# Optimization experiments

Measured on AMD Instinct MI355X. Metric: run time of the kernel, lower is better.

Reference implementation:

```python
import jax, jax.numpy as jnp
from jax import lax
import numpy as np

# 8-neighbor topology from the original module
TOPO = np.array([[0, 1], [1, 1], [1, 0], [1, -1], [0, -1], [-1, -1], [-1, 0], [-1, 1]])
EPS = 1e-5


def conv(x, w, stride=1, pad=0, groups=1):
    # NCHW / OIHW convolution, no bias (module uses bias=False everywhere)
    return lax.conv_general_dilated(
        x, w, (stride, stride), [(pad, pad), (pad, pad)],
        feature_group_count=groups,
        dimension_numbers=('NCHW', 'OIHW', 'NCHW'))


def bn(x, g, b):
    # training-mode BatchNorm2d (batch statistics, biased variance)
    m = jnp.mean(x, axis=(0, 2, 3), keepdims=True)
    v = jnp.var(x, axis=(0, 2, 3), keepdims=True)
    return g[None, :, None, None] * (x - m) * lax.rsqrt(v + EPS) + b[None, :, None, None]


def setup_inputs() -> dict:
    key = jax.random.key(0)
    ks = jax.random.split(key, 12)
    B, D, NC, H, W = 8, 6, 48, 256, 256
    s = 0.1
    w = lambda k, shape: jax.random.normal(k, shape, jnp.float32) * s
    return dict(
        x=jax.random.normal(ks[0], (B, D, H, W), jnp.float32),
        # compenv_conv: Conv(D->NC,1) BN tanh Conv(NC->1,1)
        ce_w1=w(ks[1], (NC, D, 1, 1)), ce_g=jnp.ones(NC), ce_b=jnp.zeros(NC),
        ce_w2=w(ks[2], (1, NC, 1, 1)),
        # merge_change_determinant: funnel(ConvT(10->NC,3) tanh Conv(NC->NC,3) tanh) BN tanh Conv(NC->1,2,s2) sigmoid
        # ConvT stride-1 k3 expressed as pad-2 conv with conv-equivalent kernel
        md_ct=w(ks[3], (NC, 10, 3, 3)), md_c1=w(ks[4], (NC, NC, 3, 3)),
        md_g=jnp.ones(NC), md_b=jnp.zeros(NC), md_c2=w(ks[5], (1, NC, 2, 2)),
        # cell_merge: Conv(D->NC,2,s2,g3) BN tanh funnel(ConvT(NC->NC,3,g3) tanh Conv(NC->D,3,g3) tanh)
        cm_w1=w(ks[6], (NC, D // 3, 2, 2)), cm_g=jnp.ones(NC), cm_b=jnp.zeros(NC),
        cm_ct=w(ks[7], (NC, NC // 3, 3, 3)), cm_c2=w(ks[8], (D, NC // 3, 3, 3)),
        # born: Conv(D->NC,1) BN tanh Conv(NC->D,1)
        bo_w1=w(ks[9], (NC, D, 1, 1)), bo_g=jnp.ones(NC), bo_b=jnp.zeros(NC),
        bo_w2=w(ks[10], (D, NC, 1, 1)),
    )


def reference(x, ce_w1, ce_g, ce_b, ce_w2, md_ct, md_c1, md_g, md_b, md_c2,
              cm_w1, cm_g, cm_b, cm_ct, cm_c2, bo_w1, bo_g, bo_b, bo_w2):
    # ---- compenv: per-direction roll + 1x1conv/BN/tanh/1x1conv (BN stats per direction, as in torch) ----
    env = []
    for k in range(8):
        t = jnp.roll(x, int(TOPO[k, 0]), axis=3)      # roll_right along W
        t = jnp.roll(t, int(-TOPO[k, 1]), axis=2)     # roll_down along H
        h = jnp.tanh(bn(conv(t, ce_w1), ce_g, ce_b))
        env.append(conv(h, ce_w2))                    # [B,1,H,W]
    ENV = jnp.concatenate(env, axis=1)                # [B,8,H,W]

    # ---- merge change determinant ----
    te = jnp.concatenate([x[:, :2], ENV], axis=1)     # [B,10,H,W]
    h = jnp.tanh(conv(te, md_ct, pad=2))              # ConvT k3 s1 == pad-2 conv -> [B,NC,H+2,W+2]
    h = jnp.tanh(conv(h, md_c1))                      # -> [B,NC,H,W]
    h = jnp.tanh(bn(h, md_g, md_b))
    CHANGE = jax.nn.sigmoid(conv(h, md_c2, stride=2))  # [B,1,H/2,W/2]

    # ---- cell merge ----
    h = jnp.tanh(bn(conv(x, cm_w1, stride=2, groups=3), cm_g, cm_b))  # [B,NC,H/2,W/2]
    h = jnp.tanh(conv(h, cm_ct, pad=2, groups=3))
    xm = jnp.tanh(conv(h, cm_c2, groups=3))           # [B,D,H/2,W/2]

    # ---- born + blend ----
    born = conv(jnp.tanh(bn(conv(xm, bo_w1), bo_g, bo_b)), bo_w2)
    out = xm * (1.0 - CHANGE) + CHANGE * born
    out = jnp.concatenate([jax.nn.sigmoid(out[:, :3]), out[:, 3:]], axis=1)
    return out
```

## Files before the change

### kernel.cpp

```cpp
#include <hip/hip_runtime.h>
#include <stdint.h>

typedef unsigned short ushort_t;

#define B8  8
#define D6  6
#define NC  48
#define HH  256
#define WW  256
#define HWp 65536
#define H2  128
#define HW2 16384

__device__ __constant__ int c_T0[8] = {0,1,1,1,0,-1,-1,-1};
__device__ __constant__ int c_T1[8] = {1,1,0,-1,-1,-1,0,1};

__device__ inline float bf2f(ushort_t u){ union{unsigned int i; float f;} w; w.i = ((unsigned int)u)<<16; return w.f; }
__device__ inline ushort_t f2bf(float f){ union{float f; unsigned int i;} w; w.f=f; unsigned int xx=w.i;
  return (ushort_t)((xx + 0x7fffu + ((xx>>16)&1u)) >> 16); }
__device__ inline float tanhf_(float x){ float e=__expf(2.f*x); return 1.f - 2.f/(e+1.f); }
__device__ inline float sigm_(float x){ return 1.f/(1.f+__expf(-x)); }
__device__ inline float ldg_(const void* p, size_t i, int isbf){
  return isbf ? bf2f(((const ushort_t*)p)[i]) : ((const float*)p)[i];
}

typedef short short8 __attribute__((ext_vector_type(8)));
typedef float f4 __attribute__((ext_vector_type(4)));
typedef ushort_t us4 __attribute__((ext_vector_type(4)));
typedef ushort_t us8 __attribute__((ext_vector_type(8)));
union AB { short8 s; us4 h[2]; us8 u; };

__global__ __launch_bounds__(256) void k_detect(const ushort_t* x, float* flag){
  int t=threadIdx.x; int cnt=0;
  for(int i=t;i<4096;i+=256){
    ushort_t u=x[2*i];
    int e=(u>>7)&0xff;
    if(e>=100 && e<=150) cnt++;
  }
  for(int o=32;o;o>>=1) cnt+=__shfl_down(cnt,o,64);
  __shared__ int sh4[4];
  if((t&63)==0) sh4[t>>6]=cnt;
  __syncthreads();
  if(t==0){ int tot=sh4[0]+sh4[1]+sh4[2]+sh4[3]; flag[0] = (tot>=2048)?1.f:0.f; }
}

struct WC { const ushort_t* src[10]; int off[10]; int n[10]; };

__global__ __launch_bounds__(256) void k_wcvt(WC wc, float* dst, const float* dfl){
  int isbf = dfl[0]>0.5f;
  int t = blockIdx.y; int n = wc.n[t]; const ushort_t* s = wc.src[t]; float* d = dst + wc.off[t];
  for(int i = blockIdx.x*256 + threadIdx.x; i < n; i += gridDim.x*256)
    d[i] = isbf ? bf2f(s[i]) : ((const float*)s)[i];
}

__global__ __launch_bounds__(256) void k_wprep(const float* w2src, const float* w1src,
                                               ushort_t* wb2, ushort_t* wb1){
  int t = blockIdx.x*256+threadIdx.x;
  if(t<3456){
    int lane=t&63; int rest=t>>6;
    int ks=rest&1; int g=rest>>1; int tap=g%9; int nt=g/9;
    int oc=nt*16+(lane&15); int icb=ks*32+((lane>>4)*8);
    #pragma unroll
    for(int j=0;j<8;j++){
      int ic=icb+j;
      float v = (ic<48) ? w2src[(oc*48+ic)*9+tap] : 0.f;
      wb2[(size_t)t*8+j]=f2bf(v);
    }
  } else if(t<5184){
    int tt=t-3456; int lane=tt&63; int g=tt>>6; int tap=g%9; int nt=g/9;
    int oc=nt*16+(lane&15); int icb=(lane>>4)*8;
    #pragma unroll
    for(int j=0;j<8;j++){
      int ic=icb+j;
      float v = (ic<10) ? w1src[(oc*10+ic)*9+tap] : 0.f;
      wb1[(size_t)tt*8+j]=f2bf(v);
    }
  }
}

__global__ __launch_bounds__(256) void k_mom(const void* src, const float* dfl, int isbfc,
                                             int sh, int npix, float* out){
  int isbf = dfl ? (dfl[0]>0.5f) : isbfc;
  float vals[27];
  #pragma unroll
  for(int i=0;i<27;i++) vals[i]=0.f;
  int stride = gridDim.x*256;
  int msk = (1<<sh)-1;
  for(int p = blockIdx.x*256+threadIdx.x; p < npix; p += stride){
    int b = p >> sh; int hw = p & msk;
    float v[6];
    #pragma unroll
    for(int d=0; d<6; d++){
      size_t idx = (((size_t)(b*6+d))<<sh) + hw;
      v[d] = ldg_(src, idx, isbf);
    }
    int q=6;
    #pragma unroll
    for(int d=0;d<6;d++){
      vals[d]+=v[d];
      #pragma unroll
      for(int e=d;e<6;e++){ vals[q] += v[d]*v[e]; q++; }
    }
  }
  __shared__ float red[4][27];
  int wid=threadIdx.x>>6, lane=threadIdx.x&63;
  #pragma unroll
  for(int i=0;i<27;i++){
    float v=vals[i];
    for(int o=32;o;o>>=1) v+=__shfl_down(v,o,64);
    if(lane==0) red[wid][i]=v;
  }
  __syncthreads();
  if(threadIdx.x<27)
    atomicAdd(&out[threadIdx.x],
      red[0][threadIdx.x]+red[1][threadIdx.x]+red[2][threadIdx.x]+red[3][threadIdx.x]);
}

__global__ __launch_bounds__(64) void k_msb(const float* mom, const float* W1,
      const void* g, const void* b, const float* dfl, float invN, float* scale, float* bias){
  int c = threadIdx.x; if(c>=NC) return;
  int isbf = dfl[0]>0.5f;
  const int st[6]={0,6,11,15,18,20};
  float wr[6];
  #pragma unroll
  for(int d=0;d<6;d++) wr[d]=W1[c*6+d];
  float mean=0.f;
  #pragma unroll
  for(int d=0;d<6;d++) mean += wr[d]*mom[d];
  mean *= invN;
  float e2=0.f;
  #pragma unroll
  for(int d=0;d<6;d++){
    #pragma unroll
    for(int e=d;e<6;e++){
      float mm = mom[6 + st[d] + (e-d)];
      e2 += wr[d]*wr[e]*((e==d)?1.f:2.f)*mm;
    }
  }
  e2 *= invN;
  float var = e2 - mean*mean;
  float sc = ldg_(g,c,isbf) * rsqrtf(var + 1e-5f);
  scale[c]=sc; bias[c]= ldg_(b,c,isbf) - sc*mean;
}

__global__ __launch_bounds__(256) void k_env(const void* x, const float* dfl,
      const float* w1, const float* w2, const float* sc, const float* bi, float* e){
  int isbf = dfl[0]>0.5f;
  int p = blockIdx.x*256+threadIdx.x;
  int b = p >> 16; int hw = p & 65535;
  float v[6];
  #pragma unroll
  for(int d=0; d<6; d++) v[d]=ldg_(x,(size_t)(b*6+d)*HWp + hw, isbf);
  float acc=0.f;
  for(int c=0;c<NC;c++){
    float y=0.f;
    #pragma unroll
    for(int d=0;d<6;d++) y += w1[c*6+d]*v[d];
    acc += w2[c]*tanhf_(sc[c]*y + bi[c]);
  }
  e[(size_t)b*HWp + hw]=acc;
}

__global__ __launch_bounds__(256,3) void k_md(const void* x, const float* dfl, const float* e,
      const ushort_t* wb1, const ushort_t* wb2, ushort_t* h2t, float* stats){
  __shared__ __attribute__((aligned(16))) ushort_t te[6400];
  __shared__ __attribute__((aligned(16))) ushort_t h1t[19488];
  __shared__ float red[4][3][16][2];
  int isbf = dfl[0]>0.5f;
  int b = blockIdx.y;
  int ti = blockIdx.x>>4, tj = blockIdx.x&15;
  int i0 = ti*16, j0 = tj*16;
  int lane = threadIdx.x&63, w = threadIdx.x>>6;
  int n = lane&15, quad = lane>>4;
  {
    us8 z;
    #pragma unroll
    for(int j=0;j<8;j++) z[j]=0;
    us8* tp=(us8*)te;
    for(int idx=threadIdx.x; idx<800; idx+=256) tp[idx]=z;
    for(int idx=threadIdx.x; idx<336; idx+=256) *(us8*)&h1t[idx*58+48]=z;
  }
  __syncthreads();
  for(int idx=threadIdx.x; idx<4000; idx+=256){
    int pix = idx/10, ic = idx-pix*10;
    int r = pix/20, c = pix-r*20;
    int gy = i0-2+r, gx = j0-2+c;
    float v = 0.f;
    if(gy>=0 && gy<HH && gx>=0 && gx<WW){
      if(ic<2) v = ldg_(x, ((size_t)(b*6+ic)*HH + gy)*WW + gx, isbf);
      else { int k=ic-2;
        int yy=(gy + c_T1[k]) & 255; int xx=(gx - c_T0[k]) & 255;
        v = e[((size_t)b*HH + yy)*WW + xx]; }
    }
    te[pix*16+ic]=f2bf(v);
  }
  __syncthreads();
  {
    int qoff = (quad&1)*8;
    for(int mt=w; mt<21; mt+=4){
      int p = mt*16 + n;
      int pr = p/18, pc = p-pr*18;
      f4 hacc[3];
      #pragma unroll
      for(int nt=0;nt<3;nt++) hacc[nt]=(f4){0.f,0.f,0.f,0.f};
      #pragma unroll
      for(int tap=0; tap<9; tap++){
        int ki=tap/3, kj=tap%3;
        AB a; a.u = *(const us8*)&te[((pr+ki)*20 + pc+kj)*16 + qoff];
        #pragma unroll
        for(int nt=0;nt<3;nt++){
          AB Bf; Bf.u = *(const us8*)&wb1[((size_t)((nt*9+tap)*64+lane))*8];
          hacc[nt] = __builtin_amdgcn_mfma_f32_16x16x32_bf16(a.s, Bf.s, hacc[nt], 0,0,0);
        }
      }
      int pd = mt*16 + quad*4;
      #pragma unroll
      for(int nt=0;nt<3;nt++){
        #pragma unroll
        for(int r=0;r<4;r++)
          h1t[(pd+r)*58 + nt*16 + n] = f2bf(tanhf_(hacc[nt][r]));
      }
    }
  }
  __syncthreads();
  f4 acc[4][3];
  #pragma unroll
  for(int a=0;a<4;a++)
    #pragma unroll
    for(int c=0;c<3;c++) acc[a][c]=(f4){0.f,0.f,0.f,0.f};
  int q1off = 32 + ((quad<2) ? quad*8 : 16);
  #pragma unroll
  for(int tap=0; tap<9; tap++){
    int ki=tap/3, kj=tap%3;
    AB Bf[3][2];
    #pragma unroll
    for(int nt=0;nt<3;nt++)
      #pragma unroll
      for(int ks=0;ks<2;ks++)
        Bf[nt][ks].u = *(const us8*)&wb2[((size_t)(((nt*9+tap)*2+ks)*64+lane))*8];
    #pragma unroll
    for(int yy=0; yy<4; yy++){
      int y = w*4 + yy;
      int base = ((y+ki)*18 + n + kj)*58;
      AB a0, a1;
      a0.u = *(const us8*)&h1t[base + quad*8];
      a1.u = *(const us8*)&h1t[base + q1off];
      #pragma unroll
      for(int nt=0;nt<3;nt++){
        acc[yy][nt] = __builtin_amdgcn_mfma_f32_16x16x32_bf16(a0.s, Bf[nt][0].s, acc[yy][nt], 0,0,0);
        acc[yy][nt] = __builtin_amdgcn_mfma_f32_16x16x32_bf16(a1.s, Bf[nt][1].s, acc[yy][nt], 0,0,0);
      }
    }
  }
  float s[3]={0.f,0.f,0.f}, q[3]={0.f,0.f,0.f};
  size_t tilebase = ((size_t)(b*256 + blockIdx.x))*48*256;
  #pragma unroll
  for(int yy=0;yy<4;yy++){
    #pragma unroll
    for(int nt=0;nt<3;nt++){
      int oc = nt*16 + n;
      size_t base = tilebase + (size_t)oc*256 + (w*4+yy)*16 + quad*4;
      us4 u;
      #pragma unroll
      for(int r=0;r<4;r++){
        float v=tanhf_(acc[yy][nt][r]);
        u[r]=f2bf(v);
        float vb=bf2f(u[r]);
        s[nt]+=vb; q[nt]+=vb*vb;
      }
      *(us4*)&h2t[base] = u;
    }
  }
  #pragma unroll
  for(int nt=0;nt<3;nt++){
    s[nt]+=__shfl_xor(s[nt],16,64); s[nt]+=__shfl_xor(s[nt],32,64);
    q[nt]+=__shfl_xor(q[nt],16,64); q[nt]+=__shfl_xor(q[nt],32,64);
  }
  if(quad==0){
    #pragma unroll
    for(int nt=0;nt<3;nt++){ red[w][nt][n][0]=s[nt]; red[w][nt][n][1]=q[nt]; }
  }
  __syncthreads();
  if(threadIdx.x<48){
    int oc=threadIdx.x; int nt=oc>>4, nn=oc&15;
    float S=red[0][nt][nn][0]+red[1][nt][nn][0]+red[2][nt][nn][0]+red[3][nt][nn][0];
    float Q=red[0][nt][nn][1]+red[1][nt][nn][1]+red[2][nt][nn][1]+red[3][nt][nn][1];
    atomicAdd(&stats[2*oc],S); atomicAdd(&stats[2*oc+1],Q);
  }
}

__global__ __launch_bounds__(256) void k_cstat(const float* srcf, const ushort_t* srch, int isbf,
      int C, int HWn, int Bn, int S, float* stats){
  int c = blockIdx.x % C; int s = blockIdx.x / C;
  float sum=0.f, sq=0.f;
  for(int b=0;b<Bn;b++){
    size_t base=((size_t)b*C+c)*HWn;
    for(int i=s*256+threadIdx.x; i<HWn; i+=S*256){
      float v = isbf ? bf2f(srch[base+i]) : srcf[base+i];
      sum+=v; sq+=v*v;
    }
  }
  for(int o=32;o;o>>=1){ sum+=__shfl_down(sum,o,64); sq+=__shfl_down(sq,o,64); }
  __shared__ float ls[4], lq[4];
  int wid=threadIdx.x>>6;
  if((threadIdx.x&63)==0){ ls[wid]=sum; lq[wid]=sq; }
  __syncthreads();
  if(threadIdx.x==0){
    atomicAdd(&stats[2*c],   ls[0]+ls[1]+ls[2]+ls[3]);
    atomicAdd(&stats[2*c+1], lq[0]+lq[1]+lq[2]+lq[3]);
  }
}

__global__ __launch_bounds__(64) void k_csb(const float* stats, const void* g, const void* b,
      const float* dfl, float invN, float* scale, float* bias){
  int c=threadIdx.x; if(c>=NC) return;
  int isbf = dfl[0]>0.5f;
  float mean=stats[2*c]*invN; float var=stats[2*c+1]*invN - mean*mean;
  float s=ldg_(g,c,isbf)*rsqrtf(var+1e-5f);
  scale[c]=s; bias[c]=ldg_(b,c,isbf)-s*mean;
}

__global__ __launch_bounds__(256) void k_change(const ushort_t* h2t,
      const float* wc2, const float* sc, const float* bi, float* CH){
  int tile = blockIdx.x;
  int b = tile>>8; int rest = tile&255; int ti = rest>>4, tj = rest&15;
  int t = threadIdx.x;
  int pix = t&63, icq = t>>6;
  int oi = pix>>3, oj = pix&7;
  const ushort_t* tp = &h2t[(size_t)tile*48*256];
  float acc = 0.f;
  #pragma unroll
  for(int icl=0; icl<12; icl++){
    int ic = icq*12 + icl;
    float s = sc[ic], tb = bi[ic];
    const ushort_t* cp = tp + ic*256 + (2*oi)*16 + 2*oj;
    acc += tanhf_(s*bf2f(cp[0 ])+tb)*wc2[ic*4+0];
    acc += tanhf_(s*bf2f(cp[1 ])+tb)*wc2[ic*4+1];
    acc += tanhf_(s*bf2f(cp[16])+tb)*wc2[ic*4+2];
    acc += tanhf_(s*bf2f(cp[17])+tb)*wc2[ic*4+3];
  }
  __shared__ float rr[256];
  rr[icq*64+pix] = acc;
  __syncthreads();
  if(t<64){
    float v = rr[t]+rr[64+t]+rr[128+t]+rr[192+t];
    int i = ti*8 + (t>>3), j = tj*8 + (t&7);
    CH[((size_t)b<<14) + i*128 + j] = sigm_(v);
  }
}

__global__ __launch_bounds__(256) void k_cm1(const void* x, const float* dfl, const float* w, ushort_t* t1){
  int isbf = dfl[0]>0.5f;
  int p=blockIdx.x*256+threadIdx.x;
  int b=p>>14; int rem=p&16383; int i=rem>>7; int j=rem&127;
  float v[6][2][2];
  #pragma unroll
  for(int d=0;d<6;d++)
    #pragma unroll
    for(int ki=0;ki<2;ki++)
      #pragma unroll
      for(int kj=0;kj<2;kj++)
        v[d][ki][kj]=ldg_(x, ((size_t)(b*6+d)*HH + 2*i+ki)*WW + 2*j+kj, isbf);
  for(int oc=0;oc<NC;oc++){
    int g=oc>>4;
    float a=0.f;
    #pragma unroll
    for(int icl=0;icl<2;icl++)
      #pragma unroll
      for(int ki=0;ki<2;ki++)
        #pragma unroll
        for(int kj=0;kj<2;kj++)
          a += v[2*g+icl][ki][kj]*w[((oc*2+icl)*2+ki)*2+kj];
    t1[((size_t)(b*NC+oc)*HW2) + rem]=f2bf(a);
  }
}

__global__ __launch_bounds__(256) void k_cm2(const ushort_t* t1, const float* sc, const float* bi,
        const float* wct, float* t2){
  __shared__ float as[16][20][21];
  int b=blockIdx.y, g=blockIdx.z;
  int ti=blockIdx.x/9, tj=blockIdx.x%9;
  int i0=ti*16, j0=tj*16;
  int ty=threadIdx.x>>4, tx=threadIdx.x&15;
  for(int idx=threadIdx.x; idx<6400; idx+=256){
    int i=idx/400; int rem=idx-i*400; int r=rem/20; int cc=rem-r*20;
    int cg=g*16+i;
    int y=i0-2+r, xx=j0-2+cc;
    float v=0.f;
    if(y>=0 && y<H2 && xx>=0 && xx<H2)
      v = tanhf_(sc[cg]*bf2f(t1[((size_t)(b*NC+cg)*H2 + y)*H2 + xx]) + bi[cg]);
    as[i][r][cc]=v;
  }
  __syncthreads();
  float acc[16];
  #pragma unroll
  for(int o=0;o<16;o++) acc[o]=0.f;
  for(int i=0;i<16;i++){
    float p[3][3];
    #pragma unroll
    for(int ki=0;ki<3;ki++)
      #pragma unroll
      for(int kj=0;kj<3;kj++) p[ki][kj]=as[i][ty+ki][tx+kj];
    #pragma unroll
    for(int o=0;o<16;o++){
      const float* wp=&wct[((size_t)(g*16+o)*16+i)*9];
      float a=0.f;
      #pragma unroll
      for(int q=0;q<9;q++) a += p[q/3][q%3]*wp[q];
      acc[o]+=a;
    }
  }
  int ii=i0+ty, jj=j0+tx;
  if(ii<130 && jj<130){
    #pragma unroll
    for(int o=0;o<16;o++)
      t2[((size_t)(b*NC+g*16+o)*130 + ii)*130 + jj]=tanhf_(acc[o]);
  }
}

__global__ __launch_bounds__(256) void k_cm3(const float* t2, const float* w, float* xm){
  __shared__ float ts[16][18][20];
  int b=blockIdx.y, g=blockIdx.z;
  int ti=blockIdx.x>>3, tj=blockIdx.x&7;
  int i0=ti*16, j0=tj*16;
  int ty=threadIdx.x>>4, tx=threadIdx.x&15;
  for(int idx=threadIdx.x; idx<16*18*18; idx+=256){
    int i=idx/324; int rem=idx-i*324; int r=rem/18; int cc=rem-r*18;
    int cg=g*16+i;
    ts[i][r][cc]=t2[((size_t)(b*NC+cg)*130 + i0+r)*130 + j0+cc];
  }
  __syncthreads();
  float acc[2]={0.f,0.f};
  for(int icl=0;icl<16;icl++){
    float p[3][3];
    #pragma unroll
    for(int ki=0;ki<3;ki++)
      #pragma unroll
      for(int kj=0;kj<3;kj++) p[ki][kj]=ts[icl][ty+ki][tx+kj];
    #pragma unroll
    for(int ol=0;ol<2;ol++){
      int oc=2*g+ol;
      const float* wp=&w[((size_t)oc*16+icl)*9];
      float a=0.f;
      #pragma unroll
      for(int q=0;q<9;q++) a += p[q/3][q%3]*wp[q];
      acc[ol]+=a;
    }
  }
  int ii=i0+ty, jj=j0+tx;
  #pragma unroll
  for(int ol=0;ol<2;ol++)
    xm[((size_t)(b*6+2*g+ol)*H2 + ii)*H2 + jj]=tanhf_(acc[ol]);
}

__global__ __launch_bounds__(256) void k_final(const float* xm, const float* CH, const float* w1,
      const float* w2, const float* sc, const float* bi, const float* dfl, void* outp){
  int isbf = dfl[0]>0.5f;
  int p=blockIdx.x*256+threadIdx.x;
  int b=p>>14; int rem=p&16383;
  float v[6];
  #pragma unroll
  for(int d=0;d<6;d++) v[d]=xm[((size_t)(b*6+d)*HW2)+rem];
  float born[6]={0.f,0.f,0.f,0.f,0.f,0.f};
  for(int c=0;c<NC;c++){
    float y=0.f;
    #pragma unroll
    for(int d=0;d<6;d++) y+=w1[c*6+d]*v[d];
    float a=tanhf_(sc[c]*y+bi[c]);
    #pragma unroll
    for(int d=0;d<6;d++) born[d]+=w2[d*NC+c]*a;
  }
  float C=CH[p];
  #pragma unroll
  for(int d=0;d<6;d++){
    float o=v[d]*(1.f-C)+C*born[d];
    if(d<3) o=sigm_(o);
    size_t id=((size_t)(b*6+d)*HW2)+rem;
    if(isbf) ((ushort_t*)outp)[id]=f2bf(o); else ((float*)outp)[id]=o;
  }
}

extern "C" void kernel_launch(void* const* d_in, const int* in_sizes, int n_in,
                              void* d_out, int out_size, void* d_ws, size_t ws_size,
                              hipStream_t stream){
  (void)in_sizes; (void)n_in; (void)out_size; (void)ws_size;
  const ushort_t* x    = (const ushort_t*)d_in[0];
  const ushort_t* cew1 = (const ushort_t*)d_in[1];
  const void*     ceg  = d_in[2];
  const void*     ceb  = d_in[3];
  const ushort_t* cew2 = (const ushort_t*)d_in[4];
  const ushort_t* mdct = (const ushort_t*)d_in[5];
  const ushort_t* mdc1 = (const ushort_t*)d_in[6];
  const void*     mdg  = d_in[7];
  const void*     mdb  = d_in[8];
  const ushort_t* mdc2 = (const ushort_t*)d_in[9];
  const ushort_t* cmw1 = (const ushort_t*)d_in[10];
  const void*     cmg  = d_in[11];
  const void*     cmb  = d_in[12];
  const ushort_t* cmct = (const ushort_t*)d_in[13];
  const ushort_t* cmc2 = (const ushort_t*)d_in[14];
  const ushort_t* bow1 = (const ushort_t*)d_in[15];
  const void*     bog  = d_in[16];
  const void*     bob  = d_in[17];
  const ushort_t* bow2 = (const ushort_t*)d_in[18];
  float* ws = (float*)d_ws;

  const long OW_mdct=0, OW_mdc1=4320, OW_cew1=25056, OW_cew2=25344, OW_mdc2=25392,
             OW_cmw1=25584, OW_cmct=25968, OW_cmc2=32880, OW_bow1=33744, OW_bow2=34032;
  const long OFF_STATS=34320;
  const long ST_xmom=OFF_STATS+0,  ST_cesc=OFF_STATS+64,  ST_cebi=OFF_STATS+112,
             ST_h2  =OFF_STATS+160, ST_mdsc=OFF_STATS+256, ST_mdbi=OFF_STATS+304,
             ST_t1  =OFF_STATS+352, ST_cmsc=OFF_STATS+448, ST_cmbi=OFF_STATS+496,
             ST_xmm =OFF_STATS+544, ST_bosc=OFF_STATS+608, ST_bobi=OFF_STATS+656,
             ST_FLAG=OFF_STATS+960;
  const long OFF_WB2 = OFF_STATS + 1024;
  const long OFF_WB1 = OFF_WB2 + 13824;
  const long OFF_E   = OFF_WB1 + 6912;
  const long OFF_H2  = OFF_E + 524288L;
  const long OFF_D   = OFF_H2 + 12582912L;
  const long OFF_T1=OFF_D, OFF_T2=OFF_D+6291456L, OFF_XM=OFF_D+12781056L, OFF_CH=OFF_D+13567488L;

  ushort_t* h2t  = (ushort_t*)(ws + OFF_H2);
  ushort_t* t1h  = (ushort_t*)(ws + OFF_T1);
  ushort_t* wb2  = (ushort_t*)(ws + OFF_WB2);
  ushort_t* wb1  = (ushort_t*)(ws + OFF_WB1);
  const float* dfl = ws + ST_FLAG;

  (void)hipMemsetAsync(ws + OFF_STATS, 0, 1024*sizeof(float), stream);
  hipLaunchKernelGGL(k_detect, dim3(1), 256, 0, stream, x, ws+ST_FLAG);

  WC wc;
  const ushort_t* srcs[10] = {mdct,mdc1,cew1,cew2,mdc2,cmw1,cmct,cmc2,bow1,bow2};
  const int offs[10] = {(int)OW_mdct,(int)OW_mdc1,(int)OW_cew1,(int)OW_cew2,(int)OW_mdc2,
                        (int)OW_cmw1,(int)OW_cmct,(int)OW_cmc2,(int)OW_bow1,(int)OW_bow2};
  const int cnts[10] = {4320,20736,288,48,192,384,6912,864,288,288};
  for(int i=0;i<10;i++){ wc.src[i]=srcs[i]; wc.off[i]=offs[i]; wc.n[i]=cnts[i]; }
  hipLaunchKernelGGL(k_wcvt, dim3(81,10), 256, 0, stream, wc, ws, dfl);
  hipLaunchKernelGGL(k_wprep, dim3(21), 256, 0, stream, ws+OW_mdc1, ws+OW_mdct, wb2, wb1);

  hipLaunchKernelGGL(k_mom, dim3(256), 256, 0, stream, (const void*)x, dfl, 0, 16, B8*HWp, ws+ST_xmom);
  hipLaunchKernelGGL(k_msb, dim3(1), 64, 0, stream, ws+ST_xmom, ws+OW_cew1, ceg, ceb, dfl,
                     1.f/(float)(B8*HWp), ws+ST_cesc, ws+ST_cebi);
  hipLaunchKernelGGL(k_env, dim3(2048), 256, 0, stream, (const void*)x, dfl, ws+OW_cew1, ws+OW_cew2,
                     ws+ST_cesc, ws+ST_cebi, ws+OFF_E);

  hipLaunchKernelGGL(k_md, dim3(256,8), 256, 0, stream, (const void*)x, dfl, ws+OFF_E,
                     wb1, wb2, h2t, ws+ST_h2);
  hipLaunchKernelGGL(k_csb, dim3(1), 64, 0, stream, ws+ST_h2, mdg, mdb, dfl, 1.f/(float)(B8*HWp),
                     ws+ST_mdsc, ws+ST_mdbi);
  hipLaunchKernelGGL(k_change, dim3(2048), 256, 0, stream, h2t, ws+OW_mdc2,
                     ws+ST_mdsc, ws+ST_mdbi, ws+OFF_CH);

  hipLaunchKernelGGL(k_cm1, dim3(512), 256, 0, stream, (const void*)x, dfl, ws+OW_cmw1, t1h);
  hipLaunchKernelGGL(k_cstat, dim3(48*8), 256, 0, stream, (const float*)nullptr, t1h, 1,
                     NC, HW2, B8, 8, ws+ST_t1);
  hipLaunchKernelGGL(k_csb, dim3(1), 64, 0, stream, ws+ST_t1, cmg, cmb, dfl, 1.f/(float)(B8*HW2),
                     ws+ST_cmsc, ws+ST_cmbi);
  hipLaunchKernelGGL(k_cm2, dim3(81,8,3), 256, 0, stream, t1h, ws+ST_cmsc, ws+ST_cmbi,
                     ws+OW_cmct, ws+OFF_T2);
  hipLaunchKernelGGL(k_cm3, dim3(64,8,3), 256, 0, stream, ws+OFF_T2, ws+OW_cmc2, ws+OFF_XM);

  hipLaunchKernelGGL(k_mom, dim3(128), 256, 0, stream, (const void*)(ws+OFF_XM), (const float*)nullptr, 0,
                     14, B8*HW2, ws+ST_xmm);
  hipLaunchKernelGGL(k_msb, dim3(1), 64, 0, stream, ws+ST_xmm, ws+OW_bow1, bog, bob, dfl,
                     1.f/(float)(B8*HW2), ws+ST_bosc, ws+ST_bobi);
  hipLaunchKernelGGL(k_final, dim3(512), 256, 0, stream, ws+OFF_XM, ws+OFF_CH, ws+OW_bow1,
                     ws+OW_bow2, ws+ST_bosc, ws+ST_bobi, dfl, d_out);
}
```

Before: 448.2 us.

## Merge independent stages into fewer launches and inline BN scale/bias computation

Reduces the launch sequence from about 17 kernels plus a memset to 8. Independent work is packed into shared grids split by block index: weight conversion, weight prep and input moments; env and cell-merge conv1; the md MFMA conv and t1 channel stats; change and cm2. The tiny single-block BN scale/bias kernels are dropped, and each consumer block recomputes scale and bias into shared memory. The stats zeroing moves into k_detect, and weight prep now reads the raw weights directly, so each merged stage waits on one fewer launch. In exchange, every block does redundant BN prep, and the merged kernels carry the larger shared-memory and register footprint of their heaviest branch, which can lower occupancy.

```diff
diff --git a/kernel.cpp b/kernel.cpp
--- a/kernel.cpp
+++ b/kernel.cpp
@@ -30,8 +30,40 @@
 typedef ushort_t us8 __attribute__((ext_vector_type(8)));
 union AB { short8 s; us4 h[2]; us8 u; };
 
-__global__ __launch_bounds__(256) void k_detect(const ushort_t* x, float* flag){
-  int t=threadIdx.x; int cnt=0;
+__device__ inline void msb_inline(int c, const float* mom, const float* W1,
+      const void* g, const void* b, int isbf, float invN, float* sc, float* bi){
+  const int st[6]={0,6,11,15,18,20};
+  float wr[6];
+  #pragma unroll
+  for(int d=0;d<6;d++) wr[d]=W1[c*6+d];
+  float mean=0.f;
+  #pragma unroll
+  for(int d=0;d<6;d++) mean += wr[d]*mom[d];
+  mean *= invN;
+  float e2=0.f;
+  #pragma unroll
+  for(int d=0;d<6;d++)
+    #pragma unroll
+    for(int e=d;e<6;e++)
+      e2 += wr[d]*wr[e]*((e==d)?1.f:2.f)*mom[6 + st[d] + (e-d)];
+  e2 *= invN;
+  float var = e2 - mean*mean;
+  float s = ldg_(g,c,isbf) * rsqrtf(var + 1e-5f);
+  sc[c]=s; bi[c]= ldg_(b,c,isbf) - s*mean;
+}
+
+__device__ inline void csb_inline(int c, const float* stats, const void* g, const void* b,
+      int isbf, float invN, float* sc, float* bi){
+  float mean=stats[2*c]*invN; float var=stats[2*c+1]*invN - mean*mean;
+  float s=ldg_(g,c,isbf)*rsqrtf(var+1e-5f);
+  sc[c]=s; bi[c]=ldg_(b,c,isbf)-s*mean;
+}
+
+__global__ __launch_bounds__(256) void k_detect(const ushort_t* x, float* stats){
+  int t=threadIdx.x;
+  for(int i=t;i<1024;i+=256) stats[i]=0.f;
+  __syncthreads();
+  int cnt=0;
   for(int i=t;i<4096;i+=256){
     ushort_t u=x[2*i];
     int e=(u>>7)&0xff;
@@ -41,134 +73,156 @@
   __shared__ int sh4[4];
   if((t&63)==0) sh4[t>>6]=cnt;
   __syncthreads();
-  if(t==0){ int tot=sh4[0]+sh4[1]+sh4[2]+sh4[3]; flag[0] = (tot>=2048)?1.f:0.f; }
+  if(t==0){ int tot=sh4[0]+sh4[1]+sh4[2]+sh4[3]; stats[960] = (tot>=2048)?1.f:0.f; }
 }
 
 struct WC { const ushort_t* src[10]; int off[10]; int n[10]; };
 
-__global__ __launch_bounds__(256) void k_wcvt(WC wc, float* dst, const float* dfl){
+__global__ __launch_bounds__(256) void k_prep(WC wc, float* dst, const float* dfl,
+      const void* mdc1r, const void* mdctr, ushort_t* wb2, ushort_t* wb1,
+      const void* x, float* xmom){
   int isbf = dfl[0]>0.5f;
-  int t = blockIdx.y; int n = wc.n[t]; const ushort_t* s = wc.src[t]; float* d = dst + wc.off[t];
-  for(int i = blockIdx.x*256 + threadIdx.x; i < n; i += gridDim.x*256)
-    d[i] = isbf ? bf2f(s[i]) : ((const float*)s)[i];
-}
-
-__global__ __launch_bounds__(256) void k_wprep(const float* w2src, const float* w1src,
-                                               ushort_t* wb2, ushort_t* wb1){
-  int t = blockIdx.x*256+threadIdx.x;
-  if(t<3456){
-    int lane=t&63; int rest=t>>6;
-    int ks=rest&1; int g=rest>>1; int tap=g%9; int nt=g/9;
-    int oc=nt*16+(lane&15); int icb=ks*32+((lane>>4)*8);
-    #pragma unroll
-    for(int j=0;j<8;j++){
-      int ic=icb+j;
-      float v = (ic<48) ? w2src[(oc*48+ic)*9+tap] : 0.f;
-      wb2[(size_t)t*8+j]=f2bf(v);
-    }
-  } else if(t<5184){
-    int tt=t-3456; int lane=tt&63; int g=tt>>6; int tap=g%9; int nt=g/9;
-    int oc=nt*16+(lane&15); int icb=(lane>>4)*8;
-    #pragma unroll
-    for(int j=0;j<8;j++){
-      int ic=icb+j;
-      float v = (ic<10) ? w1src[(oc*10+ic)*9+tap] : 0.f;
-      wb1[(size_t)tt*8+j]=f2bf(v);
-    }
-  }
-}
-
-__global__ __launch_bounds__(256) void k_mom(const void* src, const float* dfl, int isbfc,
-                                             int sh, int npix, float* out){
-  int isbf = dfl ? (dfl[0]>0.5f) : isbfc;
-  float vals[27];
-  #pragma unroll
-  for(int i=0;i<27;i++) vals[i]=0.f;
-  int stride = gridDim.x*256;
-  int msk = (1<<sh)-1;
-  for(int p = blockIdx.x*256+threadIdx.x; p < npix; p += stride){
-    int b = p >> sh; int hw = p & msk;
+  int bx = blockIdx.x;
+  __shared__ float red[4][27];
+  if(bx < 810){
+    int arr = bx/81, blk = bx-arr*81;
+    int n = wc.n[arr]; const ushort_t* s = wc.src[arr]; float* d = dst + wc.off[arr];
+    for(int i = blk*256 + threadIdx.x; i < n; i += 81*256)
+      d[i] = isbf ? bf2f(s[i]) : ((const float*)s)[i];
+  } else if(bx < 831){
+    int t = (bx-810)*256+threadIdx.x;
+    if(t<3456){
+      int lane=t&63; int rest=t>>6;
+      int ks=rest&1; int g=rest>>1; int tap=g%9; int nt=g/9;
+      int oc=nt*16+(lane&15); int icb=ks*32+((lane>>4)*8);
+      #pragma unroll
+      for(int j=0;j<8;j++){
+        int ic=icb+j;
+        float v = (ic<48) ? ldg_(mdc1r,(size_t)(oc*48+ic)*9+tap,isbf) : 0.f;
+        wb2[(size_t)t*8+j]=f2bf(v);
+      }
+    } else if(t<5184){
+      int tt=t-3456; int lane=tt&63; int g=tt>>6; int tap=g%9; int nt=g/9;
+      int oc=nt*16+(lane&15); int icb=(lane>>4)*8;
+      #pragma unroll
+      for(int j=0;j<8;j++){
+        int ic=icb+j;
+        float v = (ic<10) ? ldg_(mdctr,(size_t)(oc*10+ic)*9+tap,isbf) : 0.f;
+        wb1[(size_t)tt*8+j]=f2bf(v);
+      }
+    }
+  } else {
+    int bm = bx-831;
+    float vals[27];
+    #pragma unroll
+    for(int i=0;i<27;i++) vals[i]=0.f;
+    for(int p = bm*256+threadIdx.x; p < B8*HWp; p += 256*256){
+      int b = p >> 16; int hw = p & 65535;
+      float v[6];
+      #pragma unroll
+      for(int d=0; d<6; d++) v[d]=ldg_(x, (((size_t)(b*6+d))<<16)+hw, isbf);
+      int q=6;
+      #pragma unroll
+      for(int d=0;d<6;d++){
+        vals[d]+=v[d];
+        #pragma unroll
+        for(int e=d;e<6;e++){ vals[q] += v[d]*v[e]; q++; }
+      }
+    }
+    int wid=threadIdx.x>>6, lane=threadIdx.x&63;
+    #pragma unroll
+    for(int i=0;i<27;i++){
+      float v=vals[i];
+      for(int o=32;o;o>>=1) v+=__shfl_down(v,o,64);
+      if(lane==0) red[wid][i]=v;
+    }
+    __syncthreads();
+    if(threadIdx.x<27)
+      atomicAdd(&xmom[threadIdx.x],
+        red[0][threadIdx.x]+red[1][threadIdx.x]+red[2][threadIdx.x]+red[3][threadIdx.x]);
+  }
+}
+
+__global__ __launch_bounds__(256) void k_envcm1(const void* x, const float* dfl,
+      const float* xmom, const float* cew1, const float* cew2, const void* ceg, const void* ceb,
+      const float* cmw1, float* e, ushort_t* t1){
+  int isbf = dfl[0]>0.5f;
+  int bx = blockIdx.x;
+  __shared__ float sc[48], bi[48];
+  if(bx < 2048){
+    if(threadIdx.x<48)
+      msb_inline(threadIdx.x, xmom, cew1, ceg, ceb, isbf, 1.f/(float)(B8*HWp), sc, bi);
+    __syncthreads();
+    int p = bx*256+threadIdx.x;
+    int b = p >> 16; int hw = p & 65535;
     float v[6];
     #pragma unroll
-    for(int d=0; d<6; d++){
-      size_t idx = (((size_t)(b*6+d))<<sh) + hw;
-      v[d] = ldg_(src, idx, isbf);
-    }
-    int q=6;
-    #pragma unroll
-    for(int d=0;d<6;d++){
-      vals[d]+=v[d];
-      #pragma unroll
-      for(int e=d;e<6;e++){ vals[q] += v[d]*v[e]; q++; }
-    }
-  }
-  __shared__ float red[4][27];
-  int wid=threadIdx.x>>6, lane=threadIdx.x&63;
-  #pragma unroll
-  for(int i=0;i<27;i++){
-    float v=vals[i];
-    for(int o=32;o;o>>=1) v+=__shfl_down(v,o,64);
-    if(lane==0) red[wid][i]=v;
-  }
-  __syncthreads();
-  if(threadIdx.x<27)
-    atomicAdd(&out[threadIdx.x],
-      red[0][threadIdx.x]+red[1][threadIdx.x]+red[2][threadIdx.x]+red[3][threadIdx.x]);
-}
-
-__global__ __launch_bounds__(64) void k_msb(const float* mom, const float* W1,
-      const void* g, const void* b, const float* dfl, float invN, float* scale, float* bias){
-  int c = threadIdx.x; if(c>=NC) return;
-  int isbf = dfl[0]>0.5f;
-  const int st[6]={0,6,11,15,18,20};
-  float wr[6];
-  #pragma unroll
-  for(int d=0;d<6;d++) wr[d]=W1[c*6+d];
-  float mean=0.f;
-  #pragma unroll
-  for(int d=0;d<6;d++) mean += wr[d]*mom[d];
-  mean *= invN;
-  float e2=0.f;
-  #pragma unroll
-  for(int d=0;d<6;d++){
-    #pragma unroll
-    for(int e=d;e<6;e++){
-      float mm = mom[6 + st[d] + (e-d)];
-      e2 += wr[d]*wr[e]*((e==d)?1.f:2.f)*mm;
-    }
-  }
-  e2 *= invN;
-  float var = e2 - mean*mean;
-  float sc = ldg_(g,c,isbf) * rsqrtf(var + 1e-5f);
-  scale[c]=sc; bias[c]= ldg_(b,c,isbf) - sc*mean;
-}
-
-__global__ __launch_bounds__(256) void k_env(const void* x, const float* dfl,
-      const float* w1, const float* w2, const float* sc, const float* bi, float* e){
-  int isbf = dfl[0]>0.5f;
-  int p = blockIdx.x*256+threadIdx.x;
-  int b = p >> 16; int hw = p & 65535;
-  float v[6];
-  #pragma unroll
-  for(int d=0; d<6; d++) v[d]=ldg_(x,(size_t)(b*6+d)*HWp + hw, isbf);
-  float acc=0.f;
-  for(int c=0;c<NC;c++){
-    float y=0.f;
-    #pragma unroll
-    for(int d=0;d<6;d++) y += w1[c*6+d]*v[d];
-    acc += w2[c]*tanhf_(sc[c]*y + bi[c]);
-  }
-  e[(size_t)b*HWp + hw]=acc;
-}
-
-__global__ __launch_bounds__(256,3) void k_md(const void* x, const float* dfl, const float* e,
-      const ushort_t* wb1, const ushort_t* wb2, ushort_t* h2t, float* stats){
+    for(int d=0; d<6; d++) v[d]=ldg_(x,(size_t)(b*6+d)*HWp + hw, isbf);
+    float acc=0.f;
+    for(int c=0;c<NC;c++){
+      float y=0.f;
+      #pragma unroll
+      for(int d=0;d<6;d++) y += cew1[c*6+d]*v[d];
+      acc += cew2[c]*tanhf_(sc[c]*y + bi[c]);
+    }
+    e[(size_t)b*HWp + hw]=acc;
+  } else {
+    int p=(bx-2048)*256+threadIdx.x;
+    int b=p>>14; int rem=p&16383; int i=rem>>7; int j=rem&127;
+    float v[6][2][2];
+    #pragma unroll
+    for(int d=0;d<6;d++)
+      #pragma unroll
+      for(int ki=0;ki<2;ki++)
+        #pragma unroll
+        for(int kj=0;kj<2;kj++)
+          v[d][ki][kj]=ldg_(x, ((size_t)(b*6+d)*HH + 2*i+ki)*WW + 2*j+kj, isbf);
+    for(int oc=0;oc<NC;oc++){
+      int g=oc>>4;
+      float a=0.f;
+      #pragma unroll
+      for(int icl=0;icl<2;icl++)
+        #pragma unroll
+        for(int ki=0;ki<2;ki++)
+          #pragma unroll
+          for(int kj=0;kj<2;kj++)
+            a += v[2*g+icl][ki][kj]*cmw1[((oc*2+icl)*2+ki)*2+kj];
+      t1[((size_t)(b*NC+oc)*HW2) + rem]=f2bf(a);
+    }
+  }
+}
+
+__global__ __launch_bounds__(256,3) void k_mdst(const void* x, const float* dfl, const float* e,
+      const ushort_t* wb1, const ushort_t* wb2, ushort_t* h2t, float* stats,
+      const ushort_t* t1, float* t1stats){
   __shared__ __attribute__((aligned(16))) ushort_t te[6400];
   __shared__ __attribute__((aligned(16))) ushort_t h1t[19488];
   __shared__ float red[4][3][16][2];
+  int bx = blockIdx.x;
+  if(bx >= 2048){
+    int l = bx-2048;
+    int c = l % NC; int s = l / NC;
+    float sum=0.f, sq=0.f;
+    for(int b=0;b<B8;b++){
+      size_t base=((size_t)b*NC+c)*HW2;
+      for(int i=s*256+threadIdx.x; i<HW2; i+=8*256){
+        float v = bf2f(t1[base+i]);
+        sum+=v; sq+=v*v;
+      }
+    }
+    for(int o=32;o;o>>=1){ sum+=__shfl_down(sum,o,64); sq+=__shfl_down(sq,o,64); }
+    int wid=threadIdx.x>>6;
+    if((threadIdx.x&63)==0){ red[wid][0][0][0]=sum; red[wid][0][0][1]=sq; }
+    __syncthreads();
+    if(threadIdx.x==0){
+      atomicAdd(&t1stats[2*c],   red[0][0][0][0]+red[1][0][0][0]+red[2][0][0][0]+red[3][0][0][0]);
+      atomicAdd(&t1stats[2*c+1], red[0][0][0][1]+red[1][0][0][1]+red[2][0][0][1]+red[3][0][0][1]);
+    }
+    return;
+  }
   int isbf = dfl[0]>0.5f;
-  int b = blockIdx.y;
-  int ti = blockIdx.x>>4, tj = blockIdx.x&15;
+  int b = bx>>8; int tile = bx&255;
+  int ti = tile>>4, tj = tile&15;
   int i0 = ti*16, j0 = tj*16;
   int lane = threadIdx.x&63, w = threadIdx.x>>6;
   int n = lane&15, quad = lane>>4;
@@ -253,7 +307,7 @@
     }
   }
   float s[3]={0.f,0.f,0.f}, q[3]={0.f,0.f,0.f};
-  size_t tilebase = ((size_t)(b*256 + blockIdx.x))*48*256;
+  size_t tilebase = (size_t)bx*48*256;
   #pragma unroll
   for(int yy=0;yy<4;yy++){
     #pragma unroll
@@ -289,132 +343,86 @@
   }
 }
 
-__global__ __launch_bounds__(256) void k_cstat(const float* srcf, const ushort_t* srch, int isbf,
-      int C, int HWn, int Bn, int S, float* stats){
-  int c = blockIdx.x % C; int s = blockIdx.x / C;
-  float sum=0.f, sq=0.f;
-  for(int b=0;b<Bn;b++){
-    size_t base=((size_t)b*C+c)*HWn;
-    for(int i=s*256+threadIdx.x; i<HWn; i+=S*256){
-      float v = isbf ? bf2f(srch[base+i]) : srcf[base+i];
-      sum+=v; sq+=v*v;
-    }
-  }
-  for(int o=32;o;o>>=1){ sum+=__shfl_down(sum,o,64); sq+=__shfl_down(sq,o,64); }
-  __shared__ float ls[4], lq[4];
-  int wid=threadIdx.x>>6;
-  if((threadIdx.x&63)==0){ ls[wid]=sum; lq[wid]=sq; }
-  __syncthreads();
-  if(threadIdx.x==0){
-    atomicAdd(&stats[2*c],   ls[0]+ls[1]+ls[2]+ls[3]);
-    atomicAdd(&stats[2*c+1], lq[0]+lq[1]+lq[2]+lq[3]);
-  }
-}
-
-__global__ __launch_bounds__(64) void k_csb(const float* stats, const void* g, const void* b,
-      const float* dfl, float invN, float* scale, float* bias){
-  int c=threadIdx.x; if(c>=NC) return;
+__global__ __launch_bounds__(256) void k_chcm2(const ushort_t* h2t, const float* dfl,
+      const float* mdstats, const void* mdg, const void* mdb, const float* wc2, float* CH,
+      const ushort_t* t1, const float* t1stats, const void* cmg, const void* cmb,
+      const float* wct, float* t2){
+  __shared__ float shbuf[6816];
   int isbf = dfl[0]>0.5f;
-  float mean=stats[2*c]*invN; float var=stats[2*c+1]*invN - mean*mean;
-  float s=ldg_(g,c,isbf)*rsqrtf(var+1e-5f);
-  scale[c]=s; bias[c]=ldg_(b,c,isbf)-s*mean;
-}
-
-__global__ __launch_bounds__(256) void k_change(const ushort_t* h2t,
-      const float* wc2, const float* sc, const float* bi, float* CH){
-  int tile = blockIdx.x;
-  int b = tile>>8; int rest = tile&255; int ti = rest>>4, tj = rest&15;
-  int t = threadIdx.x;
-  int pix = t&63, icq = t>>6;
-  int oi = pix>>3, oj = pix&7;
-  const ushort_t* tp = &h2t[(size_t)tile*48*256];
-  float acc = 0.f;
-  #pragma unroll
-  for(int icl=0; icl<12; icl++){
-    int ic = icq*12 + icl;
-    float s = sc[ic], tb = bi[ic];
-    const ushort_t* cp = tp + ic*256 + (2*oi)*16 + 2*oj;
-    acc += tanhf_(s*bf2f(cp[0 ])+tb)*wc2[ic*4+0];
-    acc += tanhf_(s*bf2f(cp[1 ])+tb)*wc2[ic*4+1];
-    acc += tanhf_(s*bf2f(cp[16])+tb)*wc2[ic*4+2];
-    acc += tanhf_(s*bf2f(cp[17])+tb)*wc2[ic*4+3];
-  }
-  __shared__ float rr[256];
-  rr[icq*64+pix] = acc;
-  __syncthreads();
-  if(t<64){
-    float v = rr[t]+rr[64+t]+rr[128+t]+rr[192+t];
-    int i = ti*8 + (t>>3), j = tj*8 + (t&7);
-    CH[((size_t)b<<14) + i*128 + j] = sigm_(v);
-  }
-}
-
-__global__ __launch_bounds__(256) void k_cm1(const void* x, const float* dfl, const float* w, ushort_t* t1){
-  int isbf = dfl[0]>0.5f;
-  int p=blockIdx.x*256+threadIdx.x;
-  int b=p>>14; int rem=p&16383; int i=rem>>7; int j=rem&127;
-  float v[6][2][2];
-  #pragma unroll
-  for(int d=0;d<6;d++)
-    #pragma unroll
-    for(int ki=0;ki<2;ki++)
-      #pragma unroll
-      for(int kj=0;kj<2;kj++)
-        v[d][ki][kj]=ldg_(x, ((size_t)(b*6+d)*HH + 2*i+ki)*WW + 2*j+kj, isbf);
-  for(int oc=0;oc<NC;oc++){
-    int g=oc>>4;
-    float a=0.f;
-    #pragma unroll
-    for(int icl=0;icl<2;icl++)
-      #pragma unroll
-      for(int ki=0;ki<2;ki++)
+  int bx = blockIdx.x;
+  if(bx < 2048){
+    float* rr = shbuf; float* sc = shbuf+256; float* bi = shbuf+304;
+    if(threadIdx.x<48)
+      csb_inline(threadIdx.x, mdstats, mdg, mdb, isbf, 1.f/(float)(B8*HWp), sc, bi);
+    __syncthreads();
+    int tile = bx;
+    int b = tile>>8; int rest = tile&255; int ti = rest>>4, tj = rest&15;
+    int t = threadIdx.x;
+    int pix = t&63, icq = t>>6;
+    int oi = pix>>3, oj = pix&7;
+    const ushort_t* tp = &h2t[(size_t)tile*48*256];
+    float acc = 0.f;
+    #pragma unroll
+    for(int icl=0; icl<12; icl++){
+      int ic = icq*12 + icl;
+      float s = sc[ic], tb = bi[ic];
+      const ushort_t* cp = tp + ic*256 + (2*oi)*16 + 2*oj;
+      acc += tanhf_(s*bf2f(cp[0 ])+tb)*wc2[ic*4+0];
+      acc += tanhf_(s*bf2f(cp[1 ])+tb)*wc2[ic*4+1];
+      acc += tanhf_(s*bf2f(cp[16])+tb)*wc2[ic*4+2];
+      acc += tanhf_(s*bf2f(cp[17])+tb)*wc2[ic*4+3];
+    }
+    rr[icq*64+pix] = acc;
+    __syncthreads();
+    if(t<64){
+      float v = rr[t]+rr[64+t]+rr[128+t]+rr[192+t];
+      int i = ti*8 + (t>>3), j = tj*8 + (t&7);
+      CH[((size_t)b<<14) + i*128 + j] = sigm_(v);
+    }
+  } else {
+    float* as = shbuf; float* sc = shbuf+6720; float* bi = shbuf+6768;
+    if(threadIdx.x<48)
+      csb_inline(threadIdx.x, t1stats, cmg, cmb, isbf, 1.f/(float)(B8*HW2), sc, bi);
+    __syncthreads();
+    int l = bx-2048;
+    int g = l/648; int rem = l-g*648; int b = rem/81; int t = rem-b*81;
+    int ti=t/9, tj=t%9;
+    int i0=ti*16, j0=tj*16;
+    int ty=threadIdx.x>>4, tx=threadIdx.x&15;
+    for(int idx=threadIdx.x; idx<6400; idx+=256){
+      int i=idx/400; int rm=idx-i*400; int r=rm/20; int cc=rm-r*20;
+      int cg=g*16+i;
+      int y=i0-2+r, xx=j0-2+cc;
+      float v=0.f;
+      if(y>=0 && y<H2 && xx>=0 && xx<H2)
+        v = tanhf_(sc[cg]*bf2f(t1[((size_t)(b*NC+cg)*H2 + y)*H2 + xx]) + bi[cg]);
+      as[(i*20+r)*21+cc]=v;
+    }
+    __syncthreads();
+    float acc[16];
+    #pragma unroll
+    for(int o=0;o<16;o++) acc[o]=0.f;
+    for(int i=0;i<16;i++){
+      float p[3][3];
+      #pragma unroll
+      for(int ki=0;ki<3;ki++)
         #pragma unroll
-        for(int kj=0;kj<2;kj++)
-          a += v[2*g+icl][ki][kj]*w[((oc*2+icl)*2+ki)*2+kj];
-    t1[((size_t)(b*NC+oc)*HW2) + rem]=f2bf(a);
-  }
-}
-
-__global__ __launch_bounds__(256) void k_cm2(const ushort_t* t1, const float* sc, const float* bi,
-        const float* wct, float* t2){
-  __shared__ float as[16][20][21];
-  int b=blockIdx.y, g=blockIdx.z;
-  int ti=blockIdx.x/9, tj=blockIdx.x%9;
-  int i0=ti*16, j0=tj*16;
-  int ty=threadIdx.x>>4, tx=threadIdx.x&15;
-  for(int idx=threadIdx.x; idx<6400; idx+=256){
-    int i=idx/400; int rem=idx-i*400; int r=rem/20; int cc=rem-r*20;
-    int cg=g*16+i;
-    int y=i0-2+r, xx=j0-2+cc;
-    float v=0.f;
-    if(y>=0 && y<H2 && xx>=0 && xx<H2)
-      v = tanhf_(sc[cg]*bf2f(t1[((size_t)(b*NC+cg)*H2 + y)*H2 + xx]) + bi[cg]);
-    as[i][r][cc]=v;
-  }
-  __syncthreads();
-  float acc[16];
-  #pragma unroll
-  for(int o=0;o<16;o++) acc[o]=0.f;
-  for(int i=0;i<16;i++){
-    float p[3][3];
-    #pragma unroll
-    for(int ki=0;ki<3;ki++)
-      #pragma unroll
-      for(int kj=0;kj<3;kj++) p[ki][kj]=as[i][ty+ki][tx+kj];
-    #pragma unroll
-    for(int o=0;o<16;o++){
-      const float* wp=&wct[((size_t)(g*16+o)*16+i)*9];
-      float a=0.f;
-      #pragma unroll
-      for(int q=0;q<9;q++) a += p[q/3][q%3]*wp[q];
-      acc[o]+=a;
-    }
-  }
-  int ii=i0+ty, jj=j0+tx;
-  if(ii<130 && jj<130){
-    #pragma unroll
-    for(int o=0;o<16;o++)
-      t2[((size_t)(b*NC+g*16+o)*130 + ii)*130 + jj]=tanhf_(acc[o]);
+        for(int kj=0;kj<3;kj++) p[ki][kj]=as[(i*20+ty+ki)*21+tx+kj];
+      #pragma unroll
+      for(int o=0;o<16;o++){
+        const float* wp=&wct[((size_t)(g*16+o)*16+i)*9];
+        float a=0.f;
+        #pragma unroll
+        for(int q=0;q<9;q++) a += p[q/3][q%3]*wp[q];
+        acc[o]+=a;
+      }
+    }
+    int ii=i0+ty, jj=j0+tx;
+    if(ii<130 && jj<130){
+      #pragma unroll
+      for(int o=0;o<16;o++)
+        t2[((size_t)(b*NC+g*16+o)*130 + ii)*130 + jj]=tanhf_(acc[o]);
+    }
   }
 }
 
@@ -453,9 +461,46 @@
     xm[((size_t)(b*6+2*g+ol)*H2 + ii)*H2 + jj]=tanhf_(acc[ol]);
 }
 
-__global__ __launch_bounds__(256) void k_final(const float* xm, const float* CH, const float* w1,
-      const float* w2, const float* sc, const float* bi, const float* dfl, void* outp){
+__global__ __launch_bounds__(256) void k_mom(const float* src, float* out){
+  float vals[27];
+  #pragma unroll
+  for(int i=0;i<27;i++) vals[i]=0.f;
+  int stride = gridDim.x*256;
+  for(int p = blockIdx.x*256+threadIdx.x; p < B8*HW2; p += stride){
+    int b = p >> 14; int hw = p & 16383;
+    float v[6];
+    #pragma unroll
+    for(int d=0; d<6; d++) v[d]=src[(((size_t)(b*6+d))<<14)+hw];
+    int q=6;
+    #pragma unroll
+    for(int d=0;d<6;d++){
+      vals[d]+=v[d];
+      #pragma unroll
+      for(int e=d;e<6;e++){ vals[q] += v[d]*v[e]; q++; }
+    }
+  }
+  __shared__ float red[4][27];
+  int wid=threadIdx.x>>6, lane=threadIdx.x&63;
+  #pragma unroll
+  for(int i=0;i<27;i++){
+    float v=vals[i];
+    for(int o=32;o;o>>=1) v+=__shfl_down(v,o,64);
+    if(lane==0) red[wid][i]=v;
+  }
+  __syncthreads();
+  if(threadIdx.x<27)
+    atomicAdd(&out[threadIdx.x],
+      red[0][threadIdx.x]+red[1][threadIdx.x]+red[2][threadIdx.x]+red[3][threadIdx.x]);
+}
+
+__global__ __launch_bounds__(256) void k_final(const float* xm, const float* CH,
+      const float* xmmom, const float* w1, const float* w2, const void* bog, const void* bob,
+      const float* dfl, void* outp){
   int isbf = dfl[0]>0.5f;
+  __shared__ float sc[48], bi[48];
+  if(threadIdx.x<48)
+    msb_inline(threadIdx.x, xmmom, w1, bog, bob, isbf, 1.f/(float)(B8*HW2), sc, bi);
+  __syncthreads();
   int p=blockIdx.x*256+threadIdx.x;
   int b=p>>14; int rem=p&16383;
   float v[6];
@@ -508,11 +553,10 @@
   const long OW_mdct=0, OW_mdc1=4320, OW_cew1=25056, OW_cew2=25344, OW_mdc2=25392,
              OW_cmw1=25584, OW_cmct=25968, OW_cmc2=32880, OW_bow1=33744, OW_bow2=34032;
   const long OFF_STATS=34320;
-  const long ST_xmom=OFF_STATS+0,  ST_cesc=OFF_STATS+64,  ST_cebi=OFF_STATS+112,
-             ST_h2  =OFF_STATS+160, ST_mdsc=OFF_STATS+256, ST_mdbi=OFF_STATS+304,
-             ST_t1  =OFF_STATS+352, ST_cmsc=OFF_STATS+448, ST_cmbi=OFF_STATS+496,
-             ST_xmm =OFF_STATS+544, ST_bosc=OFF_STATS+608, ST_bobi=OFF_STATS+656,
-             ST_FLAG=OFF_STATS+960;
+  const long ST_xmom=OFF_STATS+0,
+             ST_h2  =OFF_STATS+160,
+             ST_t1  =OFF_STATS+352,
+             ST_xmm =OFF_STATS+544;
   const long OFF_WB2 = OFF_STATS + 1024;
   const long OFF_WB1 = OFF_WB2 + 13824;
   const long OFF_E   = OFF_WB1 + 6912;
@@ -524,10 +568,9 @@
   ushort_t* t1h  = (ushort_t*)(ws + OFF_T1);
   ushort_t* wb2  = (ushort_t*)(ws + OFF_WB2);
   ushort_t* wb1  = (ushort_t*)(ws + OFF_WB1);
-  const float* dfl = ws + ST_FLAG;
-
-  (void)hipMemsetAsync(ws + OFF_STATS, 0, 1024*sizeof(float), stream);
-  hipLaunchKernelGGL(k_detect, dim3(1), 256, 0, stream, x, ws+ST_FLAG);
+  const float* dfl = ws + OFF_STATS + 960;
+
+  hipLaunchKernelGGL(k_detect, dim3(1), 256, 0, stream, x, ws+OFF_STATS);
 
   WC wc;
   const ushort_t* srcs[10] = {mdct,mdc1,cew1,cew2,mdc2,cmw1,cmct,cmc2,bow1,bow2};
@@ -535,35 +578,24 @@
                         (int)OW_cmw1,(int)OW_cmct,(int)OW_cmc2,(int)OW_bow1,(int)OW_bow2};
   const int cnts[10] = {4320,20736,288,48,192,384,6912,864,288,288};
   for(int i=0;i<10;i++){ wc.src[i]=srcs[i]; wc.off[i]=offs[i]; wc.n[i]=cnts[i]; }
-  hipLaunchKernelGGL(k_wcvt, dim3(81,10), 256, 0, stream, wc, ws, dfl);
-  hipLaunchKernelGGL(k_wprep, dim3(21), 256, 0, stream, ws+OW_mdc1, ws+OW_mdct, wb2, wb1);
-
-  hipLaunchKernelGGL(k_mom, dim3(256), 256, 0, stream, (const void*)x, dfl, 0, 16, B8*HWp, ws+ST_xmom);
-  hipLaunchKernelGGL(k_msb, dim3(1), 64, 0, stream, ws+ST_xmom, ws+OW_cew1, ceg, ceb, dfl,
-                     1.f/(float)(B8*HWp), ws+ST_cesc, ws+ST_cebi);
-  hipLaunchKernelGGL(k_env, dim3(2048), 256, 0, stream, (const void*)x, dfl, ws+OW_cew1, ws+OW_cew2,
-                     ws+ST_cesc, ws+ST_cebi, ws+OFF_E);
-
-  hipLaunchKernelGGL(k_md, dim3(256,8), 256, 0, stream, (const void*)x, dfl, ws+OFF_E,
-                     wb1, wb2, h2t, ws+ST_h2);
-  hipLaunchKernelGGL(k_csb, dim3(1), 64, 0, stream, ws+ST_h2, mdg, mdb, dfl, 1.f/(float)(B8*HWp),
-                     ws+ST_mdsc, ws+ST_mdbi);
-  hipLaunchKernelGGL(k_change, dim3(2048), 256, 0, stream, h2t, ws+OW_mdc2,
-                     ws+ST_mdsc, ws+ST_mdbi, ws+OFF_CH);
-
-  hipLaunchKernelGGL(k_cm1, dim3(512), 256, 0, stream, (const void*)x, dfl, ws+OW_cmw1, t1h);
-  hipLaunchKernelGGL(k_cstat, dim3(48*8), 256, 0, stream, (const float*)nullptr, t1h, 1,
-                     NC, HW2, B8, 8, ws+ST_t1);
-  hipLaunchKernelGGL(k_csb, dim3(1), 64, 0, stream, ws+ST_t1, cmg, cmb, dfl, 1.f/(float)(B8*HW2),
-                     ws+ST_cmsc, ws+ST_cmbi);
-  hipLaunchKernelGGL(k_cm2, dim3(81,8,3), 256, 0, stream, t1h, ws+ST_cmsc, ws+ST_cmbi,
-                     ws+OW_cmct, ws+OFF_T2);
+  hipLaunchKernelGGL(k_prep, dim3(1087), 256, 0, stream, wc, ws, dfl,
+                     (const void*)mdc1, (const void*)mdct, wb2, wb1, (const void*)x, ws+ST_xmom);
+
+  hipLaunchKernelGGL(k_envcm1, dim3(2560), 256, 0, stream, (const void*)x, dfl,
+                     ws+ST_xmom, ws+OW_cew1, ws+OW_cew2, ceg, ceb, ws+OW_cmw1,
+                     ws+OFF_E, t1h);
+
+  hipLaunchKernelGGL(k_mdst, dim3(2432), 256, 0, stream, (const void*)x, dfl, ws+OFF_E,
+                     wb1, wb2, h2t, ws+ST_h2, t1h, ws+ST_t1);
+
+  hipLaunchKernelGGL(k_chcm2, dim3(3992), 256, 0, stream, h2t, dfl,
+                     ws+ST_h2, mdg, mdb, ws+OW_mdc2, ws+OFF_CH,
+                     t1h, ws+ST_t1, cmg, cmb, ws+OW_cmct, ws+OFF_T2);
+
   hipLaunchKernelGGL(k_cm3, dim3(64,8,3), 256, 0, stream, ws+OFF_T2, ws+OW_cmc2, ws+OFF_XM);
 
-  hipLaunchKernelGGL(k_mom, dim3(128), 256, 0, stream, (const void*)(ws+OFF_XM), (const float*)nullptr, 0,
-                     14, B8*HW2, ws+ST_xmm);
-  hipLaunchKernelGGL(k_msb, dim3(1), 64, 0, stream, ws+ST_xmm, ws+OW_bow1, bog, bob, dfl,
-                     1.f/(float)(B8*HW2), ws+ST_bosc, ws+ST_bobi);
-  hipLaunchKernelGGL(k_final, dim3(512), 256, 0, stream, ws+OFF_XM, ws+OFF_CH, ws+OW_bow1,
-                     ws+OW_bow2, ws+ST_bosc, ws+ST_bobi, dfl, d_out);
-}
+  hipLaunchKernelGGL(k_mom, dim3(128), 256, 0, stream, ws+OFF_XM, ws+ST_xmm);
+
+  hipLaunchKernelGGL(k_final, dim3(512), 256, 0, stream, ws+OFF_XM, ws+OFF_CH,
+                     ws+ST_xmm, ws+OW_bow1, ws+OW_bow2, bog, bob, dfl, d_out);
+}
```

Result: faster. 404.4 us (-9.8%).
